# Kernel tuning notes

Measured on AMD Instinct MI355X. Metric: run time of the kernel, lower is better.

## Reference

```python
import math
import jax, jax.numpy as jnp
import numpy as np

ANCHORS_SETTINGS = (
    dict(layer='p3', stride=32, size=48, scale=[2 ** (1.0 / 3.0), 2 ** (2.0 / 3.0)], aspect_ratio=[0.667, 1, 1.5]),
    dict(layer='p4', stride=64, size=96, scale=[2 ** (1.0 / 3.0), 2 ** (2.0 / 3.0)], aspect_ratio=[0.667, 1, 1.5]),
    dict(layer='p5', stride=128, size=192, scale=[1, 2 ** (1.0 / 3.0), 2 ** (2.0 / 3.0)], aspect_ratio=[0.667, 1, 1.5]),
)


def anchor_configs():
    # 21 static (kernel, stride, padding) configs, in the exact counter order of
    # weighted_anchor_aggregator (p3 x6, p4 x6, p5 x9).
    cfgs = []
    for info in ANCHORS_SETTINGS:
        stride, size = info['stride'], info['size']
        for scale in info['scale']:
            for ar in info['aspect_ratio']:
                kernel = (int(size * scale / float(ar) ** 0.5), int(size * scale * float(ar) ** 0.5))
                padding = (math.ceil((kernel[0] - stride) / 2.0), math.ceil((kernel[1] - stride) / 2.0))
                cfgs.append((kernel, (stride, stride), padding))
    return cfgs


def extract_weighted_patches(x, weights, kernel, stride, padding):
    # x: (B,H,W,C); weights: (B,k,gh,gw). Vectorized equivalent of the original
    # lax.scan over per-position dynamic_slice gathers:
    #   acc = sum_{i,j} weights[:,:,i,j] (x) x_pad[:, i*s : i*s+kh, j*s : j*s+kw, :]
    b = x.shape[0]
    _, k, gh, gw = weights.shape
    xp = jnp.pad(x, ((0, 0),
                     (padding[0], padding[0] + kernel[0]),
                     (padding[1], padding[1] + kernel[1]),
                     (0, 0)))
    rows = jnp.arange(gh)[:, None] * stride[0] + jnp.arange(kernel[0])[None, :]  # (gh, kh)
    cols = jnp.arange(gw)[:, None] * stride[1] + jnp.arange(kernel[1])[None, :]  # (gw, kw)
    # gather all strided patches: (B, gh, kh, gw, kw, C)
    patches = xp[:, rows][:, :, :, cols]
    # weighted sum over grid positions -> (B, k, kh, kw, C)
    return jnp.einsum('bkij,bihjwc->bkhwc', weights, patches)


def _aggregate(x, weights_p3, weights_p4, weights_p5):
    weights = ([weights_p3[:, a] for a in range(weights_p3.shape[1])]
               + [weights_p4[:, a] for a in range(weights_p4.shape[1])]
               + [weights_p5[:, a] for a in range(weights_p5.shape[1])])
    b, k = weights[0].shape[0], weights[0].shape[1]
    acc = jnp.zeros((b * k, 224, 224, 3), x.dtype)
    for w, (kernel, stride, padding) in zip(weights, anchor_configs()):
        agg = extract_weighted_patches(x, w, kernel, stride, padding)
        agg = agg.reshape(b * k, kernel[0], kernel[1], 3)
        acc = acc + jax.image.resize(agg, (b * k, 224, 224, 3), 'bilinear')
    return acc


def setup_inputs() -> dict:
    key = jax.random.key(0)
    k0, k1, k2, k3 = jax.random.split(key, 4)
    B, K = 8, 4
    return {
        'x': jax.random.normal(k0, (B, 448, 448, 3), jnp.float32),
        'weights_p3': jax.random.uniform(k1, (B, 6, K, 14, 14), jnp.float32),
        'weights_p4': jax.random.uniform(k2, (B, 6, K, 7, 7), jnp.float32),
        'weights_p5': jax.random.uniform(k3, (B, 9, K, 4, 4), jnp.float32),
    }


def reference(x, weights_p3, weights_p4, weights_p5):
    return _aggregate(x, weights_p3, weights_p4, weights_p5)
```

## Files before the change

kernel.cpp:

```cpp
#include <hip/hip_runtime.h>
#include <math.h>


#define BATCH 8
#define KK 4
#define OUT_HW 224
#define IMG_HW 448
#define NCFG 21

#define WTBL_BYTES (NCFG * 2 * OUT_HW * 16)
#define ITBL_BYTES (NCFG * 2 * OUT_HW * 4)
#define WT_OFF_BYTES (WTBL_BYTES + ITBL_BYTES)
#define WT_F4 12912
#define AGG_OFF_BYTES (WT_OFF_BYTES + WT_F4 * 16)

typedef float v2f __attribute__((ext_vector_type(2)));

static constexpr int cKH[NCFG]  = {74,60,49,93,76,62, 148,120,98,186,152,124,
                                   235,192,156,296,241,197,373,304,248};
static constexpr int cKW[NCFG]  = {49,60,74,62,76,93, 98,120,148,124,152,186,
                                   156,192,235,197,241,296,248,304,373};
static constexpr int cMTH[NCFG] = {2,2,2,2,2,2, 2,2,2,2,2,2, 3,2,2,3,3,2,4,3,3};
static constexpr int cMTW[NCFG] = {2,2,2,2,2,2, 2,2,2,2,2,2, 2,2,3,2,3,3,3,3,4};

__host__ __device__ constexpr int ckwp(int c) { return cKW[c] + (cKW[c] & 1); }
__host__ __device__ constexpr long cwsoff(int c, int g) {
    long o = 0;
    for (int k = g; k < c; ++k) o += (long)cKH[k] * ckwp(k) * (BATCH * KK);
    return o;
}

struct ACfg {
    int kh, kw, kwp, p0, p1;
    int layer;
    int qpr;
    int wt_off;
    int ws_off;
    int block_start;
    int blocks_per_img;
};

struct AggArgs {
    ACfg e[NCFG];
    int n;
};

struct TablesArgs { int kh[NCFG]; int kw[NCFG]; };

struct TrArgs {
    int layer[NCFG];
    int anchor[NCFG];
    int gsz[NCFG];
    int wt_off[NCFG];
};

struct F3 { float a, b, c; };

__device__ inline unsigned int bf16_rne(float f) {
    unsigned int u = __float_as_uint(f);
    return (u + 0x7fffu + ((u >> 16) & 1u)) >> 16;
}

__global__ __launch_bounds__(256) void init_tables(float4* __restrict__ wtbl,
                                                   int* __restrict__ itbl,
                                                   TablesArgs t) {
    int cfg = blockIdx.x >> 1;
    int dim = blockIdx.x & 1;
    int o = threadIdx.x;
    if (o >= OUT_HW) return;
    int n = dim ? t.kw[cfg] : t.kh[cfg];

    float inv = (float)(1.0 / ((double)OUT_HW / (double)n));
    float ks  = inv > 1.f ? inv : 1.f;
    float rks = 1.f / ks;
    float sf  = ((float)o + 0.5f) * inv - 0.5f;
    int i0 = (int)ceilf(sf - ks);  if (i0 < 0) i0 = 0;
    int i1 = (int)floorf(sf + ks); if (i1 > n - 1) i1 = n - 1;
    float sum = 0.f;
    for (int i = i0; i <= i1; ++i) {
        float v = 1.f - fabsf((float)i - sf) * rks;
        sum += (v > 0.f ? v : 0.f);
    }
    float rsum = 1.f / sum;
    float w[4];
#pragma unroll
    for (int d = 0; d < 4; ++d) {
        int i = i0 + d;
        float v = 0.f;
        if (i <= i1) {
            v = 1.f - fabsf((float)i - sf) * rks;
            v = (v > 0.f ? v : 0.f) * rsum;
        }
        w[d] = v;
    }
    int idx = cfg * (2 * OUT_HW) + dim * OUT_HW + o;
    wtbl[idx] = make_float4(w[0], w[1], w[2], w[3]);
    itbl[idx] = i0;
}

__global__ __launch_bounds__(256) void transpose_w(
        const float* __restrict__ wp3, const float* __restrict__ wp4,
        const float* __restrict__ wp5, float4* __restrict__ wT, TrArgs t) {
    int cfg = blockIdx.x;
    int b = blockIdx.y;
    int gsz = t.gsz[cfg];
    const float* base;
    int A;
    if (t.layer[cfg] == 0)      { base = wp3; A = 6; }
    else if (t.layer[cfg] == 1) { base = wp4; A = 6; }
    else                        { base = wp5; A = 9; }
    const float* src = base + (size_t)(b * A + t.anchor[cfg]) * (KK * gsz);
    for (int g = threadIdx.x; g < gsz; g += 256) {
        wT[t.wt_off[cfg] + b * gsz + g] =
            make_float4(src[0 * gsz + g], src[1 * gsz + g],
                        src[2 * gsz + g], src[3 * gsz + g]);
    }
}

template <int GH, int GW, int STRIDE>
__device__ inline void agg_body(const ACfg& c, int b, int h, int w0,
                                const float* __restrict__ xb,
                                const float4* __restrict__ wlds,
                                uint2* __restrict__ agg) {
    v2f acc2[4][3];
#pragma unroll
    for (int k = 0; k < 4; ++k)
#pragma unroll
        for (int ch = 0; ch < 3; ++ch) { acc2[k][ch].x = 0.f; acc2[k][ch].y = 0.f; }

    const int rb = h - c.p0;
    int ilo = rb >= 0 ? 0 : (-rb + STRIDE - 1) / STRIDE;
    int ihi = (IMG_HW - 1 - rb) / STRIDE;
    if (ihi > GH - 1) ihi = GH - 1;

    const int cb = w0 - c.p1;

#pragma unroll 1
    for (int i = ilo; i <= ihi; ++i) {
        const float* xr = xb + (size_t)(rb + i * STRIDE) * (IMG_HW * 3);
        const float4* wrow = wlds + i * GW;
#pragma unroll
        for (int j = 0; j < GW; ++j) {
            int col = cb + j * STRIDE;
            unsigned cc0 = (unsigned)col;
            if (cc0 > (unsigned)(IMG_HW - 1)) cc0 = (unsigned)(IMG_HW - 1);
            unsigned cc1 = (unsigned)(col + 1);
            if (cc1 > (unsigned)(IMG_HW - 1)) cc1 = (unsigned)(IMG_HW - 1);
            F3 v0 = *(const F3*)(xr + (size_t)cc0 * 3);
            F3 v1 = *(const F3*)(xr + (size_t)cc1 * 3);
            bool k0 = (unsigned)col < (unsigned)IMG_HW;
            bool k1 = (unsigned)(col + 1) < (unsigned)IMG_HW;
            v2f d0, d1, d2;
            d0.x = k0 ? v0.a : 0.f;  d0.y = k1 ? v1.a : 0.f;
            d1.x = k0 ? v0.b : 0.f;  d1.y = k1 ? v1.b : 0.f;
            d2.x = k0 ? v0.c : 0.f;  d2.y = k1 ? v1.c : 0.f;
            float4 wk = wrow[j];
            v2f wv0 = {wk.x, wk.x};
            v2f wv1 = {wk.y, wk.y};
            v2f wv2 = {wk.z, wk.z};
            v2f wv3 = {wk.w, wk.w};
            acc2[0][0] = __builtin_elementwise_fma(wv0, d0, acc2[0][0]);
            acc2[0][1] = __builtin_elementwise_fma(wv0, d1, acc2[0][1]);
            acc2[0][2] = __builtin_elementwise_fma(wv0, d2, acc2[0][2]);
            acc2[1][0] = __builtin_elementwise_fma(wv1, d0, acc2[1][0]);
            acc2[1][1] = __builtin_elementwise_fma(wv1, d1, acc2[1][1]);
            acc2[1][2] = __builtin_elementwise_fma(wv1, d2, acc2[1][2]);
            acc2[2][0] = __builtin_elementwise_fma(wv2, d0, acc2[2][0]);
            acc2[2][1] = __builtin_elementwise_fma(wv2, d1, acc2[2][1]);
            acc2[2][2] = __builtin_elementwise_fma(wv2, d2, acc2[2][2]);
            acc2[3][0] = __builtin_elementwise_fma(wv3, d0, acc2[3][0]);
            acc2[3][1] = __builtin_elementwise_fma(wv3, d1, acc2[3][1]);
            acc2[3][2] = __builtin_elementwise_fma(wv3, d2, acc2[3][2]);
        }
    }

    const int npix = c.kh * c.kwp;
#pragma unroll
    for (int k = 0; k < 4; ++k) {
        size_t base = (size_t)c.ws_off + (size_t)(b * KK + k) * npix
                    + (size_t)h * c.kwp + w0;
        uint4 o;
        o.x = bf16_rne(acc2[k][0].x) | (bf16_rne(acc2[k][1].x) << 16);
        o.y = bf16_rne(acc2[k][2].x);
        o.z = bf16_rne(acc2[k][0].y) | (bf16_rne(acc2[k][1].y) << 16);
        o.w = bf16_rne(acc2[k][2].y);
        *(uint4*)(agg + base) = o;
    }
}

__global__ __launch_bounds__(256, 4) void agg_all(
        const float* __restrict__ x,
        const float4* __restrict__ wT,
        uint2* __restrict__ agg,
        AggArgs a) {
    int bid = blockIdx.x;
    int ci = 0;
    while (ci + 1 < a.n && bid >= a.e[ci + 1].block_start) ci++;
    const ACfg c = a.e[ci];
    int local = bid - c.block_start;
    int b     = local & 7;
    int sblk  = local >> 3;

    const int gsz = (c.layer == 0) ? 196 : (c.layer == 1) ? 49 : 16;
    __shared__ float4 wlds[196];
    for (int t = threadIdx.x; t < gsz; t += 256)
        wlds[t] = wT[c.wt_off + b * gsz + t];
    __syncthreads();

    int pidx = sblk * 256 + (int)threadIdx.x;
    if (pidx >= c.kh * c.qpr) return;
    int h  = pidx / c.qpr;
    int w0 = (pidx - h * c.qpr) * 2;

    const float* __restrict__ xb = x + (size_t)b * (IMG_HW * IMG_HW * 3);
    if (c.layer == 0)      agg_body<14, 14, 32>(c, b, h, w0, xb, wlds, agg);
    else if (c.layer == 1) agg_body<7, 7, 64>(c, b, h, w0, xb, wlds, agg);
    else                   agg_body<4, 4, 128>(c, b, h, w0, xb, wlds, agg);
}

template <int TH, int TW, int KH_, int KW_, int KWP_>
__device__ inline void taps_ct(const uint2* __restrict__ base,
                               int i0, int j0,
                               float4 wh4, float4 ww4,
                               float& a0, float& a1, float& a2) {
    const float* wh = (const float*)&wh4;
    const float* ww = (const float*)&ww4;
    uint2 v[TH][TW];
#pragma unroll
    for (int d = 0; d < TH; ++d) {
        int gi = i0 + d;
        if (gi > KH_ - 1) gi = KH_ - 1;
        const uint2* rp = base + (size_t)gi * KWP_;
#pragma unroll
        for (int e = 0; e < TW; ++e) {
            int gj = j0 + e;
            if (gj > KW_ - 1) gj = KW_ - 1;
            v[d][e] = rp[gj];
        }
    }
#pragma unroll
    for (int d = 0; d < TH; ++d) {
        float r0 = 0.f, r1 = 0.f, r2 = 0.f;
#pragma unroll
        for (int e = 0; e < TW; ++e) {
            uint2 t = v[d][e];
            float c0 = __uint_as_float(t.x << 16);
            float c1 = __uint_as_float(t.x & 0xffff0000u);
            float c2 = __uint_as_float(t.y << 16);
            float w = ww[e];
            r0 = fmaf(w, c0, r0);
            r1 = fmaf(w, c1, r1);
            r2 = fmaf(w, c2, r2);
        }
        a0 = fmaf(wh[d], r0, a0);
        a1 = fmaf(wh[d], r1, a1);
        a2 = fmaf(wh[d], r2, a2);
    }
}

template <int C, int CEND, int CSTART>
__device__ inline void do_rounds(const uint2* __restrict__ agg,
                                 const float4* __restrict__ wlds,
                                 const int* __restrict__ ilds,
                                 int bk, int tx, int ty,
                                 float& a0, float& a1, float& a2) {
    if constexpr (C < CEND) {
        constexpr int li  = C - CSTART;
        constexpr int kh  = cKH[C];
        constexpr int kw  = cKW[C];
        constexpr int kwp = ckwp(C);
        constexpr long wso = cwsoff(C, CSTART);
        float4 wh4 = wlds[li * 32 + ty];
        float4 ww4 = wlds[li * 32 + 16 + tx];
        int i0 = ilds[li * 32 + ty];
        int j0 = ilds[li * 32 + 16 + tx];
        const uint2* plane = agg + wso + (size_t)bk * (kh * kwp);
        taps_ct<cMTH[C], cMTW[C], kh, kw, kwp>(plane, i0, j0, wh4, ww4,
                                               a0, a1, a2);
        do_rounds<C + 1, CEND, CSTART>(agg, wlds, ilds, bk, tx, ty,
                                       a0, a1, a2);
    }
}

template <int CSTART, int CEND>
__global__ __launch_bounds__(256, 4) void resize_static(
        const uint2* __restrict__ agg,
        const float4* __restrict__ wtbl,
        const int* __restrict__ itbl,
        float* __restrict__ out,
        int accumulate) {
    constexpr int NC = CEND - CSTART;
    const int tid = threadIdx.x;
    const int tx = tid & 15;
    const int ty = tid >> 4;
    const int xo = blockIdx.x * 16 + tx;
    const int yo = blockIdx.y * 16 + ty;
    const int bk = blockIdx.z;

    __shared__ float4 wlds[NC * 32];
    __shared__ int    ilds[NC * 32];

    for (int e = tid; e < NC * 32; e += 256) {
        int ci  = e >> 5;
        int r   = e & 31;
        int isW = r >> 4;
        int idx = r & 15;
        int base_o = isW ? (blockIdx.x * 16) : (blockIdx.y * 16);
        int src = (CSTART + ci) * (2 * OUT_HW) + isW * OUT_HW + base_o + idx;
        wlds[ci * 32 + r] = wtbl[src];
        ilds[ci * 32 + r] = itbl[src];
    }
    __syncthreads();

    size_t ob = (((size_t)bk * OUT_HW + yo) * OUT_HW + xo) * 3;
    float a0, a1, a2;
    if (accumulate) {
        a0 = out[ob]; a1 = out[ob + 1]; a2 = out[ob + 2];
    } else {
        a0 = a1 = a2 = 0.f;
    }

    do_rounds<CSTART, CEND, CSTART>(agg, wlds, ilds, bk, tx, ty, a0, a1, a2);

    out[ob + 0] = a0; out[ob + 1] = a1; out[ob + 2] = a2;
}

extern "C" void kernel_launch(void* const* d_in, const int* in_sizes, int n_in,
                              void* d_out, int out_size, void* d_ws, size_t ws_size,
                              hipStream_t stream) {
    const float* x   = (const float*)d_in[0];
    const float* wp3 = (const float*)d_in[1];
    const float* wp4 = (const float*)d_in[2];
    const float* wp5 = (const float*)d_in[3];
    float* out = (float*)d_out;
    float4* wtbl = (float4*)d_ws;
    int*    itbl = (int*)((char*)d_ws + WTBL_BYTES);
    float4* wT   = (float4*)((char*)d_ws + WT_OFF_BYTES);
    uint2*  agg  = (uint2*)((char*)d_ws + AGG_OFF_BYTES);

    struct { int stride, size, nscale; double scales[3]; int gh; } layers[3] = {
        {32, 48, 2, {pow(2.0, 1.0 / 3.0), pow(2.0, 2.0 / 3.0), 0.0}, 14},
        {64, 96, 2, {pow(2.0, 1.0 / 3.0), pow(2.0, 2.0 / 3.0), 0.0}, 7},
        {128, 192, 3, {1.0, pow(2.0, 1.0 / 3.0), pow(2.0, 2.0 / 3.0)}, 4},
    };
    const double ars[3] = {0.667, 1.0, 1.5};

    struct HostCfg {
        int kh, kw, kwp, stride, p0, p1, gh, gw, layer, anchor, wt_off;
        int qpr, blocks_per_img;
    } cfg[NCFG];
    TablesArgs ta;
    TrArgs tr;
    int nc = 0, wt_run = 0;
    for (int L = 0; L < 3; ++L) {
        int anchor = 0;
        for (int si = 0; si < layers[L].nscale; ++si) {
            for (int ai = 0; ai < 3; ++ai) {
                double ss = (double)layers[L].size * layers[L].scales[si];
                double sq = pow(ars[ai], 0.5);
                int kh = (int)(ss / sq);
                int kw = (int)(ss * sq);
                HostCfg& e = cfg[nc];
                e.kh = kh; e.kw = kw;
                e.kwp = kw + (kw & 1);
                e.stride = layers[L].stride;
                e.p0 = (int)ceil((double)(kh - layers[L].stride) / 2.0);
                e.p1 = (int)ceil((double)(kw - layers[L].stride) / 2.0);
                e.gh = layers[L].gh; e.gw = layers[L].gh;
                e.layer = L; e.anchor = anchor++;
                e.qpr = e.kwp / 2;
                e.blocks_per_img = (kh * e.qpr + 255) / 256;
                e.wt_off = wt_run;
                int gsz = e.gh * e.gw;
                wt_run += BATCH * gsz;
                ta.kh[nc] = kh; ta.kw[nc] = kw;
                tr.layer[nc] = L; tr.anchor[nc] = e.anchor;
                tr.gsz[nc] = gsz; tr.wt_off[nc] = e.wt_off;
                ++nc;
            }
        }
    }

    init_tables<<<NCFG * 2, 256, 0, stream>>>(wtbl, itbl, ta);
    transpose_w<<<dim3(NCFG, BATCH), 256, 0, stream>>>(wp3, wp4, wp5, wT, tr);

    dim3 rgrid(OUT_HW / 16, OUT_HW / 16, BATCH * KK);

    auto build = [&](int gstart, int gend, AggArgs& aa) -> int {
        aa.n = 0;
        int ablocks = 0;
        size_t off = 0;
        for (int c = gstart; c < gend; ++c) {
            ACfg& lc = aa.e[aa.n++];
            lc.kh = cfg[c].kh; lc.kw = cfg[c].kw; lc.kwp = cfg[c].kwp;
            lc.p0 = cfg[c].p0; lc.p1 = cfg[c].p1;
            lc.layer = cfg[c].layer;
            lc.qpr = cfg[c].qpr;
            lc.wt_off = cfg[c].wt_off;
            lc.ws_off = (int)off;
            lc.block_start = ablocks;
            lc.blocks_per_img = cfg[c].blocks_per_img;
            ablocks += cfg[c].blocks_per_img * BATCH;
            off += (size_t)cfg[c].kh * cfg[c].kwp * (BATCH * KK);
        }
        return ablocks;
    };

    AggArgs aa;
    int nb;

    nb = build(0, 15, aa);
    agg_all<<<nb, 256, 0, stream>>>(x, wT, agg, aa);
    resize_static<0, 15><<<rgrid, 256, 0, stream>>>(agg, wtbl, itbl, out, 0);

    nb = build(15, 19, aa);
    agg_all<<<nb, 256, 0, stream>>>(x, wT, agg, aa);
    resize_static<15, 19><<<rgrid, 256, 0, stream>>>(agg, wtbl, itbl, out, 1);

    nb = build(19, 21, aa);
    agg_all<<<nb, 256, 0, stream>>>(x, wT, agg, aa);
    resize_static<19, 21><<<rgrid, 256, 0, stream>>>(agg, wtbl, itbl, out, 1);

    (void)in_sizes; (void)n_in; (void)out_size; (void)ws_size;
}
```

Baseline: 275.5 us.

## Make resize separable with LDS-staged source tile and 32x8 output blocks

The resize kernel now stages each block's source tile of the aggregated patch in shared memory. It applies the vertical antialias taps first into per-row temporaries, then the horizontal taps. This replaces per-pixel gathers of the full 2D tap footprint from global memory. Output blocks change from 16x16 to 32x8, and per-pixel weights and indices are read straight from global tables. The cost is three barriers per config and more LDS use.

```diff
diff --git a/kernel.cpp b/kernel.cpp
--- a/kernel.cpp
+++ b/kernel.cpp
@@ -29,6 +29,15 @@
     for (int k = g; k < c; ++k) o += (long)cKH[k] * ckwp(k) * (BATCH * KK);
     return o;
 }
+__host__ __device__ constexpr int cRmax(int c) {
+    return (8 * cKH[c] + 223) / 224 + cMTH[c] + 1;
+}
+__host__ __device__ constexpr int cCmax(int c) {
+    return (32 * cKW[c] + 223) / 224 + cMTW[c] + 1;
+}
+
+#define A_MAX 832
+#define T_W   64
 
 struct ACfg {
     int kh, kw, kwp, p0, p1;
@@ -218,99 +227,102 @@
     else                   agg_body<4, 4, 128>(c, b, h, w0, xb, wlds, agg);
 }
 
-template <int TH, int TW, int KH_, int KW_, int KWP_>
-__device__ inline void taps_ct(const uint2* __restrict__ base,
-                               int i0, int j0,
-                               float4 wh4, float4 ww4,
-                               float& a0, float& a1, float& a2) {
-    const float* wh = (const float*)&wh4;
-    const float* ww = (const float*)&ww4;
-    uint2 v[TH][TW];
-#pragma unroll
-    for (int d = 0; d < TH; ++d) {
-        int gi = i0 + d;
-        if (gi > KH_ - 1) gi = KH_ - 1;
-        const uint2* rp = base + (size_t)gi * KWP_;
-#pragma unroll
-        for (int e = 0; e < TW; ++e) {
-            int gj = j0 + e;
-            if (gj > KW_ - 1) gj = KW_ - 1;
-            v[d][e] = rp[gj];
-        }
-    }
-#pragma unroll
-    for (int d = 0; d < TH; ++d) {
-        float r0 = 0.f, r1 = 0.f, r2 = 0.f;
-#pragma unroll
-        for (int e = 0; e < TW; ++e) {
-            uint2 t = v[d][e];
-            float c0 = __uint_as_float(t.x << 16);
-            float c1 = __uint_as_float(t.x & 0xffff0000u);
-            float c2 = __uint_as_float(t.y << 16);
-            float w = ww[e];
-            r0 = fmaf(w, c0, r0);
-            r1 = fmaf(w, c1, r1);
-            r2 = fmaf(w, c2, r2);
-        }
-        a0 = fmaf(wh[d], r0, a0);
-        a1 = fmaf(wh[d], r1, a1);
-        a2 = fmaf(wh[d], r2, a2);
-    }
-}
-
 template <int C, int CEND, int CSTART>
-__device__ inline void do_rounds(const uint2* __restrict__ agg,
-                                 const float4* __restrict__ wlds,
-                                 const int* __restrict__ ilds,
-                                 int bk, int tx, int ty,
-                                 float& a0, float& a1, float& a2) {
+__device__ inline void sep_rounds(const uint2* __restrict__ agg,
+                                  const float4* __restrict__ wtbl,
+                                  const int* __restrict__ itbl,
+                                  uint2* __restrict__ lds_a,
+                                  float (*tmpR)[T_W], float (*tmpG)[T_W],
+                                  float (*tmpB)[T_W],
+                                  int bk, int tx, int ty, int xo, int yo,
+                                  float& a0, float& a1, float& a2) {
     if constexpr (C < CEND) {
-        constexpr int li  = C - CSTART;
         constexpr int kh  = cKH[C];
         constexpr int kw  = cKW[C];
         constexpr int kwp = ckwp(C);
+        constexpr int mth = cMTH[C];
+        constexpr int mtw = cMTW[C];
+        constexpr int R   = cRmax(C);
+        constexpr int CW  = cCmax(C);
         constexpr long wso = cwsoff(C, CSTART);
-        float4 wh4 = wlds[li * 32 + ty];
-        float4 ww4 = wlds[li * 32 + 16 + tx];
-        int i0 = ilds[li * 32 + ty];
-        int j0 = ilds[li * 32 + 16 + tx];
+        const int tid = ty * 32 + tx;
+
         const uint2* plane = agg + wso + (size_t)bk * (kh * kwp);
-        taps_ct<cMTH[C], cMTW[C], kh, kw, kwp>(plane, i0, j0, wh4, ww4,
-                                               a0, a1, a2);
-        do_rounds<C + 1, CEND, CSTART>(agg, wlds, ilds, bk, tx, ty,
-                                       a0, a1, a2);
+        const int ri0 = itbl[C * (2 * OUT_HW) + blockIdx.y * 8];
+        const int ci0 = itbl[C * (2 * OUT_HW) + OUT_HW + blockIdx.x * 32];
+        float4 wh4 = wtbl[C * (2 * OUT_HW) + yo];
+        float4 ww4 = wtbl[C * (2 * OUT_HW) + OUT_HW + xo];
+        const int i0 = itbl[C * (2 * OUT_HW) + yo];
+        const int j0 = itbl[C * (2 * OUT_HW) + OUT_HW + xo];
+        const float* wh = (const float*)&wh4;
+        const float* ww = (const float*)&ww4;
+
+#pragma unroll
+        for (int p = tid; p < R * CW; p += 256) {
+            int r  = p / CW;
+            int cc = p - r * CW;
+            int gr = ri0 + r; if (gr > kh - 1) gr = kh - 1;
+            int gc = ci0 + cc; if (gc > kw - 1) gc = kw - 1;
+            lds_a[p] = plane[(size_t)gr * kwp + gc];
+        }
+        __syncthreads();
+
+        {
+            int lr = i0 - ri0;
+#pragma unroll
+            for (int cc = tx; cc < CW; cc += 32) {
+                float t0 = 0.f, t1 = 0.f, t2 = 0.f;
+#pragma unroll
+                for (int d = 0; d < mth; ++d) {
+                    uint2 u = lds_a[(lr + d) * CW + cc];
+                    float w = wh[d];
+                    t0 = fmaf(w, __uint_as_float(u.x << 16), t0);
+                    t1 = fmaf(w, __uint_as_float(u.x & 0xffff0000u), t1);
+                    t2 = fmaf(w, __uint_as_float(u.y << 16), t2);
+                }
+                tmpR[ty][cc] = t0;
+                tmpG[ty][cc] = t1;
+                tmpB[ty][cc] = t2;
+            }
+        }
+        __syncthreads();
+
+        {
+            int lc = j0 - ci0;
+#pragma unroll
+            for (int e = 0; e < mtw; ++e) {
+                float w = ww[e];
+                a0 = fmaf(w, tmpR[ty][lc + e], a0);
+                a1 = fmaf(w, tmpG[ty][lc + e], a1);
+                a2 = fmaf(w, tmpB[ty][lc + e], a2);
+            }
+        }
+        __syncthreads();
+
+        sep_rounds<C + 1, CEND, CSTART>(agg, wtbl, itbl, lds_a,
+                                        tmpR, tmpG, tmpB,
+                                        bk, tx, ty, xo, yo, a0, a1, a2);
     }
 }
 
 template <int CSTART, int CEND>
-__global__ __launch_bounds__(256, 4) void resize_static(
+__global__ __launch_bounds__(256, 4) void resize_sep(
         const uint2* __restrict__ agg,
         const float4* __restrict__ wtbl,
         const int* __restrict__ itbl,
         float* __restrict__ out,
         int accumulate) {
-    constexpr int NC = CEND - CSTART;
     const int tid = threadIdx.x;
-    const int tx = tid & 15;
-    const int ty = tid >> 4;
-    const int xo = blockIdx.x * 16 + tx;
-    const int yo = blockIdx.y * 16 + ty;
+    const int tx = tid & 31;
+    const int ty = tid >> 5;
+    const int xo = blockIdx.x * 32 + tx;
+    const int yo = blockIdx.y * 8 + ty;
     const int bk = blockIdx.z;
 
-    __shared__ float4 wlds[NC * 32];
-    __shared__ int    ilds[NC * 32];
-
-    for (int e = tid; e < NC * 32; e += 256) {
-        int ci  = e >> 5;
-        int r   = e & 31;
-        int isW = r >> 4;
-        int idx = r & 15;
-        int base_o = isW ? (blockIdx.x * 16) : (blockIdx.y * 16);
-        int src = (CSTART + ci) * (2 * OUT_HW) + isW * OUT_HW + base_o + idx;
-        wlds[ci * 32 + r] = wtbl[src];
-        ilds[ci * 32 + r] = itbl[src];
-    }
-    __syncthreads();
+    __shared__ uint2 lds_a[A_MAX];
+    __shared__ float tmpR[8][T_W];
+    __shared__ float tmpG[8][T_W];
+    __shared__ float tmpB[8][T_W];
 
     size_t ob = (((size_t)bk * OUT_HW + yo) * OUT_HW + xo) * 3;
     float a0, a1, a2;
@@ -320,7 +332,9 @@
         a0 = a1 = a2 = 0.f;
     }
 
-    do_rounds<CSTART, CEND, CSTART>(agg, wlds, ilds, bk, tx, ty, a0, a1, a2);
+    sep_rounds<CSTART, CEND, CSTART>(agg, wtbl, itbl, lds_a,
+                                     tmpR, tmpG, tmpB,
+                                     bk, tx, ty, xo, yo, a0, a1, a2);
 
     out[ob + 0] = a0; out[ob + 1] = a1; out[ob + 2] = a2;
 }
@@ -384,7 +398,7 @@
     init_tables<<<NCFG * 2, 256, 0, stream>>>(wtbl, itbl, ta);
     transpose_w<<<dim3(NCFG, BATCH), 256, 0, stream>>>(wp3, wp4, wp5, wT, tr);
 
-    dim3 rgrid(OUT_HW / 16, OUT_HW / 16, BATCH * KK);
+    dim3 rgrid(OUT_HW / 32, OUT_HW / 8, BATCH * KK);
 
     auto build = [&](int gstart, int gend, AggArgs& aa) -> int {
         aa.n = 0;
@@ -411,15 +425,15 @@
 
     nb = build(0, 15, aa);
     agg_all<<<nb, 256, 0, stream>>>(x, wT, agg, aa);
-    resize_static<0, 15><<<rgrid, 256, 0, stream>>>(agg, wtbl, itbl, out, 0);
+    resize_sep<0, 15><<<rgrid, 256, 0, stream>>>(agg, wtbl, itbl, out, 0);
 
     nb = build(15, 19, aa);
     agg_all<<<nb, 256, 0, stream>>>(x, wT, agg, aa);
-    resize_static<15, 19><<<rgrid, 256, 0, stream>>>(agg, wtbl, itbl, out, 1);
+    resize_sep<15, 19><<<rgrid, 256, 0, stream>>>(agg, wtbl, itbl, out, 1);
 
     nb = build(19, 21, aa);
     agg_all<<<nb, 256, 0, stream>>>(x, wT, agg, aa);
-    resize_static<19, 21><<<rgrid, 256, 0, stream>>>(agg, wtbl, itbl, out, 1);
+    resize_sep<19, 21><<<rgrid, 256, 0, stream>>>(agg, wtbl, itbl, out, 1);
 
     (void)in_sizes; (void)n_in; (void)out_size; (void)ws_size;
 }
```

New measurement: 325.4 us. 18.1% more time.

## Pair output columns a stride apart to share input pixel loads

Applied to the files above, without the earlier changes.

Each thread now computes two output columns separated by the grid stride instead of two adjacent columns, so the GW+1 input pixels loaded per row cover both outputs and each load is reused by neighbouring grid taps. This roughly halves the input gathers per FMA in the aggregation kernel. The per-thread column offsets and bounds checks are hoisted out of the row loop. In exchange it raises register pressure (launch bounds lowered from 4 to 3 blocks per SM), uses a conditional second store, and writes two separate 8-byte stores rather than one 16-byte store.

```diff
diff --git a/kernel.cpp b/kernel.cpp
--- a/kernel.cpp
+++ b/kernel.cpp
@@ -33,7 +33,7 @@
 struct ACfg {
     int kh, kw, kwp, p0, p1;
     int layer;
-    int qpr;
+    int ns;
     int wt_off;
     int ws_off;
     int block_start;
@@ -117,11 +117,15 @@
     }
 }
 
-template <int GH, int GW, int STRIDE>
-__device__ inline void agg_body(const ACfg& c, int b, int h, int w0,
+template <int GH, int GW, int STRIDE, int L2S>
+__device__ inline void agg_body(const ACfg& c, int b, int h, int slot,
                                 const float* __restrict__ xb,
                                 const float4* __restrict__ wlds,
                                 uint2* __restrict__ agg) {
+    const int w0 = (((slot >> L2S) << (L2S + 1)) | (slot & (STRIDE - 1)));
+    const int w1 = w0 + STRIDE;
+    const bool two = w1 < c.kw;
+
     v2f acc2[4][3];
 #pragma unroll
     for (int k = 0; k < 4; ++k)
@@ -135,26 +139,37 @@
 
     const int cb = w0 - c.p1;
 
+    int  cof[GW + 1];
+    bool ok [GW + 1];
+#pragma unroll
+    for (int jj = 0; jj <= GW; ++jj) {
+        int col = cb + jj * STRIDE;
+        ok[jj] = (unsigned)col < (unsigned)IMG_HW;
+        unsigned cc = (unsigned)col;
+        if (cc > (unsigned)(IMG_HW - 1)) cc = (unsigned)(IMG_HW - 1);
+        cof[jj] = (int)cc * 3;
+    }
+
 #pragma unroll 1
     for (int i = ilo; i <= ihi; ++i) {
         const float* xr = xb + (size_t)(rb + i * STRIDE) * (IMG_HW * 3);
         const float4* wrow = wlds + i * GW;
+
+        float px[GW + 1][3];
+#pragma unroll
+        for (int jj = 0; jj <= GW; ++jj) {
+            F3 v = *(const F3*)(xr + cof[jj]);
+            px[jj][0] = ok[jj] ? v.a : 0.f;
+            px[jj][1] = ok[jj] ? v.b : 0.f;
+            px[jj][2] = ok[jj] ? v.c : 0.f;
+        }
+
 #pragma unroll
         for (int j = 0; j < GW; ++j) {
-            int col = cb + j * STRIDE;
-            unsigned cc0 = (unsigned)col;
-            if (cc0 > (unsigned)(IMG_HW - 1)) cc0 = (unsigned)(IMG_HW - 1);
-            unsigned cc1 = (unsigned)(col + 1);
-            if (cc1 > (unsigned)(IMG_HW - 1)) cc1 = (unsigned)(IMG_HW - 1);
-            F3 v0 = *(const F3*)(xr + (size_t)cc0 * 3);
-            F3 v1 = *(const F3*)(xr + (size_t)cc1 * 3);
-            bool k0 = (unsigned)col < (unsigned)IMG_HW;
-            bool k1 = (unsigned)(col + 1) < (unsigned)IMG_HW;
-            v2f d0, d1, d2;
-            d0.x = k0 ? v0.a : 0.f;  d0.y = k1 ? v1.a : 0.f;
-            d1.x = k0 ? v0.b : 0.f;  d1.y = k1 ? v1.b : 0.f;
-            d2.x = k0 ? v0.c : 0.f;  d2.y = k1 ? v1.c : 0.f;
             float4 wk = wrow[j];
+            v2f d0 = {px[j][0], px[j + 1][0]};
+            v2f d1 = {px[j][1], px[j + 1][1]};
+            v2f d2 = {px[j][2], px[j + 1][2]};
             v2f wv0 = {wk.x, wk.x};
             v2f wv1 = {wk.y, wk.y};
             v2f wv2 = {wk.z, wk.z};
@@ -179,16 +194,20 @@
     for (int k = 0; k < 4; ++k) {
         size_t base = (size_t)c.ws_off + (size_t)(b * KK + k) * npix
                     + (size_t)h * c.kwp + w0;
-        uint4 o;
-        o.x = bf16_rne(acc2[k][0].x) | (bf16_rne(acc2[k][1].x) << 16);
-        o.y = bf16_rne(acc2[k][2].x);
-        o.z = bf16_rne(acc2[k][0].y) | (bf16_rne(acc2[k][1].y) << 16);
-        o.w = bf16_rne(acc2[k][2].y);
-        *(uint4*)(agg + base) = o;
-    }
-}
-
-__global__ __launch_bounds__(256, 4) void agg_all(
+        uint2 o0;
+        o0.x = bf16_rne(acc2[k][0].x) | (bf16_rne(acc2[k][1].x) << 16);
+        o0.y = bf16_rne(acc2[k][2].x);
+        agg[base] = o0;
+        if (two) {
+            uint2 o1;
+            o1.x = bf16_rne(acc2[k][0].y) | (bf16_rne(acc2[k][1].y) << 16);
+            o1.y = bf16_rne(acc2[k][2].y);
+            agg[base + STRIDE] = o1;
+        }
+    }
+}
+
+__global__ __launch_bounds__(256, 3) void agg_all(
         const float* __restrict__ x,
         const float4* __restrict__ wT,
         uint2* __restrict__ agg,
@@ -208,14 +227,14 @@
     __syncthreads();
 
     int pidx = sblk * 256 + (int)threadIdx.x;
-    if (pidx >= c.kh * c.qpr) return;
-    int h  = pidx / c.qpr;
-    int w0 = (pidx - h * c.qpr) * 2;
+    if (pidx >= c.kh * c.ns) return;
+    int h    = pidx / c.ns;
+    int slot = pidx - h * c.ns;
 
     const float* __restrict__ xb = x + (size_t)b * (IMG_HW * IMG_HW * 3);
-    if (c.layer == 0)      agg_body<14, 14, 32>(c, b, h, w0, xb, wlds, agg);
-    else if (c.layer == 1) agg_body<7, 7, 64>(c, b, h, w0, xb, wlds, agg);
-    else                   agg_body<4, 4, 128>(c, b, h, w0, xb, wlds, agg);
+    if (c.layer == 0)      agg_body<14, 14, 32, 5>(c, b, h, slot, xb, wlds, agg);
+    else if (c.layer == 1) agg_body<7, 7, 64, 6>(c, b, h, slot, xb, wlds, agg);
+    else                   agg_body<4, 4, 128, 7>(c, b, h, slot, xb, wlds, agg);
 }
 
 template <int TH, int TW, int KH_, int KW_, int KWP_>
@@ -347,7 +366,7 @@
 
     struct HostCfg {
         int kh, kw, kwp, stride, p0, p1, gh, gw, layer, anchor, wt_off;
-        int qpr, blocks_per_img;
+        int ns, blocks_per_img;
     } cfg[NCFG];
     TablesArgs ta;
     TrArgs tr;
@@ -368,8 +387,10 @@
                 e.p1 = (int)ceil((double)(kw - layers[L].stride) / 2.0);
                 e.gh = layers[L].gh; e.gw = layers[L].gh;
                 e.layer = L; e.anchor = anchor++;
-                e.qpr = e.kwp / 2;
-                e.blocks_per_img = (kh * e.qpr + 255) / 256;
+                int s = e.stride;
+                int q = kw / s, r = kw % s;
+                e.ns = ((q + 1) / 2) * s + ((q % 2 == 0) ? r : 0);
+                e.blocks_per_img = (kh * e.ns + 255) / 256;
                 e.wt_off = wt_run;
                 int gsz = e.gh * e.gw;
                 wt_run += BATCH * gsz;
@@ -395,7 +416,7 @@
             lc.kh = cfg[c].kh; lc.kw = cfg[c].kw; lc.kwp = cfg[c].kwp;
             lc.p0 = cfg[c].p0; lc.p1 = cfg[c].p1;
             lc.layer = cfg[c].layer;
-            lc.qpr = cfg[c].qpr;
+            lc.ns = cfg[c].ns;
             lc.wt_off = cfg[c].wt_off;
             lc.ws_off = (int)off;
             lc.block_start = ablocks;
```

Result: no change. 271.9 us (-1.3%).
